# Optimization experiments

Hardware: AMD Instinct MI355X
Metric: run time of the kernel (lower is better)

Reference implementation:

```python
import jax, jax.numpy as jnp
import numpy as np

B, T, D, H = 32, 1024, 512, 512


def setup_inputs() -> dict:
    key = jax.random.key(0)
    ks = jax.random.split(key, 9)
    K = 1.0 / np.sqrt(H)
    u = lambda k, s: jax.random.uniform(k, s, jnp.float32, -K, K)
    return {
        "x": jax.random.normal(ks[0], (B, T, D), jnp.float32),
        "w_ih_fw": u(ks[1], (3 * H, D)),
        "w_hh_fw": u(ks[2], (3 * H, H)),
        "b_ih_fw": u(ks[3], (3 * H,)),
        "b_hh_fw": u(ks[4], (3 * H,)),
        "w_ih_bw": u(ks[5], (3 * H, D)),
        "w_hh_bw": u(ks[6], (3 * H, H)),
        "b_ih_bw": u(ks[7], (3 * H,)),
        "b_hh_bw": u(ks[8], (3 * H,)),
    }


def _gru_scan(x, w_ih, w_hh, b_ih, b_hh, reverse):
    # x: (B, T, D) -> precompute input projections for all steps: (T, B, 3H)
    b, t, d = x.shape
    h_dim = w_hh.shape[1]
    ih = jnp.einsum("btd,gd->tbg", x, w_ih) + b_ih

    def step(h, ih_t):
        hh = h @ w_hh.T + b_hh  # (B, 3H)
        r = jax.nn.sigmoid(ih_t[:, :h_dim] + hh[:, :h_dim])
        z = jax.nn.sigmoid(ih_t[:, h_dim:2 * h_dim] + hh[:, h_dim:2 * h_dim])
        n = jnp.tanh(ih_t[:, 2 * h_dim:] + r * hh[:, 2 * h_dim:])
        h_new = (1.0 - z) * n + z * h
        return h_new, h_new

    h0 = jnp.zeros((b, h_dim), x.dtype)
    h_last, ys = jax.lax.scan(step, h0, ih, reverse=reverse)
    # ys: (T, B, H), aligned to original time indices even when reverse=True
    return jnp.transpose(ys, (1, 0, 2)), h_last


def reference(x, w_ih_fw, w_hh_fw, b_ih_fw, b_hh_fw, w_ih_bw, w_hh_bw, b_ih_bw, b_hh_bw):
    out_fw, h_fw = _gru_scan(x, w_ih_fw, w_hh_fw, b_ih_fw, b_hh_fw, reverse=False)
    out_bw, h_bw = _gru_scan(x, w_ih_bw, w_hh_bw, b_ih_bw, b_hh_bw, reverse=True)
    outputs = jnp.concatenate([out_fw, out_bw], axis=-1)  # (B, T, 2H)
    return outputs, h_fw, h_bw
```

## Files before the change

kernel.cpp:

```cpp
#include <hip/hip_runtime.h>


#define T_LEN 1024
#define B_SZ  32
#define D_SZ  512
#define H_SZ  512
#define NWG_DIR 32
#define JW 16
#define NTHR 512

typedef __attribute__((ext_vector_type(8))) _Float16 half8;
typedef __attribute__((ext_vector_type(4))) float f32x4;
typedef __attribute__((ext_vector_type(4))) int int4v;

__device__ __forceinline__ _Float16 f2h(float f) { return (_Float16)f; }
__device__ __forceinline__ float sigm_f(float v) {
  return __builtin_amdgcn_rcpf(1.f + __expf(-v));
}
__device__ __forceinline__ float tanh_f(float v) {
  return 1.f - 2.f * __builtin_amdgcn_rcpf(1.f + __expf(2.f * v));
}
__device__ __forceinline__ void bar_lgkm() {
  asm volatile("s_waitcnt lgkmcnt(0)\ns_barrier" ::: "memory");
}

__global__ __launch_bounds__(NTHR, 2)
void gru2_persistent(const float* __restrict__ x,
                     const float* __restrict__ wih_fw, const float* __restrict__ whh_fw,
                     const float* __restrict__ bih_fw, const float* __restrict__ bhh_fw,
                     const float* __restrict__ wih_bw, const float* __restrict__ whh_bw,
                     const float* __restrict__ bih_bw, const float* __restrict__ bhh_bw,
                     float* __restrict__ out,
                     unsigned* __restrict__ hexu,
                     unsigned* __restrict__ flags,
                     unsigned* __restrict__ xcdmap,
                     unsigned* __restrict__ gbar,
                     unsigned* __restrict__ slowCnt)
{
  const int bid = blockIdx.x;
  const int dir = bid & 7;
  if (dir >= 2) return;
  const int g = bid >> 3;

  __shared__ float Cp[24 * 272];
  __shared__ float biasLds[96];
  __shared__ int fastSh;

  const int tid  = threadIdx.x;
  const int wave = tid >> 6;
  const int lane = tid & 63;

  const float* wih = dir ? wih_bw : wih_fw;
  const float* whh = dir ? whh_bw : whh_fw;
  const float* bih = dir ? bih_bw : bih_fw;
  const float* bhh = dir ? bhh_bw : bhh_fw;

  if (tid < 48) {
    int grow = (tid >> 4) * H_SZ + g * JW + (tid & 15);
    biasLds[tid]      = bih[grow];
    biasLds[48 + tid] = bhh[grow];
  }

  {
    unsigned xcc;
    asm volatile("s_getreg_b32 %0, hwreg(20, 0, 32)" : "=s"(xcc));
    if (tid == 0)
      __hip_atomic_store(&xcdmap[dir * NWG_DIR + g], xcc + 1u,
                         __ATOMIC_RELAXED, __HIP_MEMORY_SCOPE_AGENT);
    if (wave == 0) {
      unsigned v = 0u; int bud = 1 << 17; bool ok = true;
      for (;;) {
        v = __hip_atomic_load(&xcdmap[lane], __ATOMIC_RELAXED,
                              __HIP_MEMORY_SCOPE_AGENT);
        if (__all(v != 0u)) break;
        if (--bud < 0) { ok = false; break; }
        __builtin_amdgcn_s_sleep(8);
      }
      const unsigned ref0 = __shfl(v, 0);
      const unsigned ref1 = __shfl(v, NWG_DIR);
      const bool uni = __all((lane < NWG_DIR) ? (v == ref0) : (v == ref1));
      if (lane == 0) fastSh = (ok && uni && ref0 != ref1) ? 1 : 0;
    }
  }
  __syncthreads();
  __builtin_amdgcn_fence(__ATOMIC_ACQUIRE, "agent");
  __syncthreads();

  if (tid == 0) {
    if (!fastSh)
      __hip_atomic_fetch_add(slowCnt, 1u, __ATOMIC_RELAXED,
                             __HIP_MEMORY_SCOPE_AGENT);
    asm volatile("s_waitcnt vmcnt(0)" ::: "memory");
    __hip_atomic_fetch_add(gbar, 1u, __ATOMIC_RELAXED, __HIP_MEMORY_SCOPE_AGENT);
    int bud = 1 << 18; bool arrived = true;
    while (__hip_atomic_load(gbar, __ATOMIC_RELAXED,
                             __HIP_MEMORY_SCOPE_AGENT) < 64u) {
      if (--bud < 0) { arrived = false; break; }
      __builtin_amdgcn_s_sleep(4);
    }
    unsigned sv = __hip_atomic_load(slowCnt, __ATOMIC_RELAXED,
                                    __HIP_MEMORY_SCOPE_AGENT);
    fastSh = (arrived && sv == 0u && fastSh) ? 1 : 0;
  }
  __syncthreads();
  const bool fast = (fastSh != 0);

  const bool isHh = (wave >= 4);
  const int  wv   = wave & 3;
  const int  wm   = wv & 1;
  const int  kh   = wv >> 1;

  half8 Bf[3][8];
  {
    const float* W = isHh ? whh : wih;
    #pragma unroll
    for (int gam = 0; gam < 3; ++gam) {
      const int row = gam * H_SZ + g * JW + (lane & 15);
      #pragma unroll
      for (int i = 0; i < 8; ++i) {
        const float* src = W + (size_t)row * D_SZ + (kh * 8 + i) * 32 + ((lane >> 4) << 3);
        float4 v0 = *(const float4*)(src);
        float4 v1 = *(const float4*)(src + 4);
        half8 b;
        b[0]=f2h(v0.x); b[1]=f2h(v0.y); b[2]=f2h(v0.z); b[3]=f2h(v0.w);
        b[4]=f2h(v1.x); b[5]=f2h(v1.y); b[6]=f2h(v1.z); b[7]=f2h(v1.w);
        Bf[gam][i] = b;
      }
    }
  }

  const int arow = wm * 16 + (lane & 15);
  const int koff = (lane >> 4) << 3;
  const float* const xwavebase = x + (size_t)arow * T_LEN * D_SZ + kh * 256 + koff;

  float4 xn[16];
  if (!isHh) {
    const int t0 = dir ? (T_LEN - 1) : 0;
    const float* base = xwavebase + (size_t)t0 * D_SZ;
    #pragma unroll
    for (int i = 0; i < 8; ++i) {
      xn[2*i]   = *(const float4*)(base + i * 32);
      xn[2*i+1] = *(const float4*)(base + i * 32 + 4);
    }
  }
  __syncthreads();

  float hreg = 0.f;
  const int gb = tid >> 4;
  const int gj = tid & 15;
  float* hlast = out + (size_t)B_SZ * T_LEN * (2 * H_SZ) + (size_t)dir * B_SZ * H_SZ;
  const unsigned* const fa = flags + (size_t)dir * NWG_DIR + kh * 16 + (lane & 15);
  int pollbud = 1 << 21;

  for (int s = 0; s < T_LEN; ++s) {
    const int t = dir ? (T_LEN - 1 - s) : s;
    const bool hasNext = (s + 1 < T_LEN);

    f32x4 acc[3] = {{0.f,0.f,0.f,0.f},{0.f,0.f,0.f,0.f},{0.f,0.f,0.f,0.f}};

    if (!isHh) {
      half8 a[8];
      #pragma unroll
      for (int i = 0; i < 8; ++i) {
        float4 u = xn[2*i], w = xn[2*i+1];
        half8 h;
        h[0]=f2h(u.x); h[1]=f2h(u.y); h[2]=f2h(u.z); h[3]=f2h(u.w);
        h[4]=f2h(w.x); h[5]=f2h(w.y); h[6]=f2h(w.z); h[7]=f2h(w.w);
        a[i] = h;
      }
      #pragma unroll
      for (int i = 0; i < 8; ++i)
        #pragma unroll
        for (int gam = 0; gam < 3; ++gam)
          acc[gam] = __builtin_amdgcn_mfma_f32_16x16x32_f16(a[i], Bf[gam][i], acc[gam], 0, 0, 0);
    } else if (s > 0) {
      if (fast) {
        {
          unsigned va, vb;
          asm volatile("global_load_dword %0, %1, off sc0" : "=&v"(va) : "v"(fa));
          asm volatile("global_load_dword %0, %1, off sc0" : "=&v"(vb) : "v"(fa));
          for (;;) {
            asm volatile("s_waitcnt vmcnt(1)" ::: "memory");
            if (__all(va >= (unsigned)s)) break;
            if (--pollbud < 0) break;
            asm volatile("global_load_dword %0, %1, off sc0" : "=&v"(va) : "v"(fa));
            asm volatile("s_waitcnt vmcnt(1)" ::: "memory");
            if (__all(vb >= (unsigned)s)) break;
            if (--pollbud < 0) break;
            asm volatile("global_load_dword %0, %1, off sc0" : "=&v"(vb) : "v"(fa));
          }
          asm volatile("s_waitcnt vmcnt(0)" ::: "memory");
        }
        const char* p0 = (const char*)hexu
            + (((size_t)dir * 2 + ((s - 1) & 1)) * (B_SZ * (H_SZ / 2))) * 4
            + (size_t)arow * (H_SZ * 2) + (size_t)(kh * 256 + koff) * 2;
        int4v hv[8];
        asm volatile(
          "global_load_dwordx4 %0, %8, off sc0\n\t"
          "global_load_dwordx4 %1, %8, off offset:64 sc0\n\t"
          "global_load_dwordx4 %2, %8, off offset:128 sc0\n\t"
          "global_load_dwordx4 %3, %8, off offset:192 sc0\n\t"
          "global_load_dwordx4 %4, %8, off offset:256 sc0\n\t"
          "global_load_dwordx4 %5, %8, off offset:320 sc0\n\t"
          "global_load_dwordx4 %6, %8, off offset:384 sc0\n\t"
          "global_load_dwordx4 %7, %8, off offset:448 sc0\n\t"
          "s_waitcnt vmcnt(0)"
          : "=&v"(hv[0]), "=&v"(hv[1]), "=&v"(hv[2]), "=&v"(hv[3]),
            "=&v"(hv[4]), "=&v"(hv[5]), "=&v"(hv[6]), "=&v"(hv[7])
          : "v"(p0) : "memory");
        __builtin_amdgcn_sched_barrier(0);
        #pragma unroll
        for (int i = 0; i < 8; ++i) {
          half8 a = __builtin_bit_cast(half8, hv[i]);
          #pragma unroll
          for (int gam = 0; gam < 3; ++gam)
            acc[gam] = __builtin_amdgcn_mfma_f32_16x16x32_f16(a, Bf[gam][i], acc[gam], 0, 0, 0);
        }
      } else {
        {
          unsigned va, vb;
          asm volatile("global_load_dword %0, %1, off sc0 sc1" : "=&v"(va) : "v"(fa));
          asm volatile("global_load_dword %0, %1, off sc0 sc1" : "=&v"(vb) : "v"(fa));
          for (;;) {
            asm volatile("s_waitcnt vmcnt(1)" ::: "memory");
            if (__all(va >= (unsigned)s)) break;
            if (--pollbud < 0) break;
            asm volatile("global_load_dword %0, %1, off sc0 sc1" : "=&v"(va) : "v"(fa));
            asm volatile("s_waitcnt vmcnt(1)" ::: "memory");
            if (__all(vb >= (unsigned)s)) break;
            if (--pollbud < 0) break;
            asm volatile("global_load_dword %0, %1, off sc0 sc1" : "=&v"(vb) : "v"(fa));
          }
          asm volatile("s_waitcnt vmcnt(0)" ::: "memory");
        }
        const char* p0 = (const char*)hexu
            + (((size_t)dir * 2 + ((s - 1) & 1)) * (B_SZ * (H_SZ / 2))) * 4
            + (size_t)arow * (H_SZ * 2) + (size_t)(kh * 256 + koff) * 2;
        int4v hv[8];
        asm volatile(
          "global_load_dwordx4 %0, %8, off sc0 sc1\n\t"
          "global_load_dwordx4 %1, %8, off offset:64 sc0 sc1\n\t"
          "global_load_dwordx4 %2, %8, off offset:128 sc0 sc1\n\t"
          "global_load_dwordx4 %3, %8, off offset:192 sc0 sc1\n\t"
          "global_load_dwordx4 %4, %8, off offset:256 sc0 sc1\n\t"
          "global_load_dwordx4 %5, %8, off offset:320 sc0 sc1\n\t"
          "global_load_dwordx4 %6, %8, off offset:384 sc0 sc1\n\t"
          "global_load_dwordx4 %7, %8, off offset:448 sc0 sc1\n\t"
          "s_waitcnt vmcnt(0)"
          : "=&v"(hv[0]), "=&v"(hv[1]), "=&v"(hv[2]), "=&v"(hv[3]),
            "=&v"(hv[4]), "=&v"(hv[5]), "=&v"(hv[6]), "=&v"(hv[7])
          : "v"(p0) : "memory");
        __builtin_amdgcn_sched_barrier(0);
        #pragma unroll
        for (int i = 0; i < 8; ++i) {
          half8 a = __builtin_bit_cast(half8, hv[i]);
          #pragma unroll
          for (int gam = 0; gam < 3; ++gam)
            acc[gam] = __builtin_amdgcn_mfma_f32_16x16x32_f16(a, Bf[gam][i], acc[gam], 0, 0, 0);
        }
      }
    }

    {
      const int src = isHh ? 1 : 0;
      #pragma unroll
      for (int gam = 0; gam < 3; ++gam) {
        float* cp = Cp + (size_t)(((src*2 + kh)*3 + gam)*2 + wm) * 272
                       + ((lane >> 4) << 2) * 17 + (lane & 15);
        #pragma unroll
        for (int vv2 = 0; vv2 < 4; ++vv2) cp[vv2 * 17] = acc[gam][vv2];
      }
    }
    bar_lgkm();

    float hnS;
    {
      const int mb = gb >> 4, rb = gb & 15;
      float sih[3], shh[3];
      #pragma unroll
      for (int gam = 0; gam < 3; ++gam) {
        float aih = 0.f, ahh = 0.f;
        #pragma unroll
        for (int q = 0; q < 2; ++q) {
          aih += Cp[(size_t)(((0*2+q)*3+gam)*2 + mb) * 272 + rb * 17 + gj];
          ahh += Cp[(size_t)(((1*2+q)*3+gam)*2 + mb) * 272 + rb * 17 + gj];
        }
        sih[gam] = aih + biasLds[gam * 16 + gj];
        shh[gam] = ahh + biasLds[48 + gam * 16 + gj];
      }
      const float r = sigm_f(sih[0] + shh[0]);
      const float z = sigm_f(sih[1] + shh[1]);
      const float n = tanh_f(sih[2] + r * shh[2]);
      const float hn = (1.f - z) * n + z * hreg;
      hreg = hn;
      hnS = hn;

      const float hother = __shfl_xor(hn, 1);
      if ((gj & 1) == 0) {
        union { unsigned u; _Float16 h[2]; } pr;
        pr.h[0] = f2h(hn); pr.h[1] = f2h(hother);
        unsigned* hp = hexu + ((size_t)dir * 2 + (s & 1)) * (B_SZ * (H_SZ / 2))
                     + (size_t)gb * (H_SZ / 2) + (g * JW + gj) / 2;
        if (fast)
          asm volatile("global_store_dword %0, %1, off sc0"
                       :: "v"(hp), "v"(pr.u) : "memory");
        else
          __hip_atomic_store(hp, pr.u, __ATOMIC_RELAXED, __HIP_MEMORY_SCOPE_AGENT);
      }
    }
    asm volatile("s_waitcnt vmcnt(0)" ::: "memory");
    bar_lgkm();
    if (tid == 0) {
      unsigned* fp = flags + (size_t)dir * NWG_DIR + g;
      const unsigned fv = (unsigned)(s + 1);
      if (fast)
        asm volatile("global_store_dword %0, %1, off sc0"
                     :: "v"(fp), "v"(fv) : "memory");
      else
        __hip_atomic_store(fp, fv, __ATOMIC_RELAXED, __HIP_MEMORY_SCOPE_AGENT);
    }

    out[((size_t)gb * T_LEN + t) * (2 * H_SZ) + dir * H_SZ + g * JW + gj] = hnS;
    if (s == T_LEN - 1) hlast[gb * H_SZ + g * JW + gj] = hnS;
    if (!isHh && hasNext) {
      const int tn = dir ? (T_LEN - 2 - s) : (s + 1);
      const float* base = xwavebase + (size_t)tn * D_SZ;
      #pragma unroll
      for (int i = 0; i < 8; ++i) {
        xn[2*i]   = *(const float4*)(base + i * 32);
        xn[2*i+1] = *(const float4*)(base + i * 32 + 4);
      }
    }
  }

  __builtin_amdgcn_fence(__ATOMIC_RELEASE, "agent");
}

extern "C" void kernel_launch(void* const* d_in, const int* in_sizes, int n_in,
                              void* d_out, int out_size, void* d_ws, size_t ws_size,
                              hipStream_t stream) {
  const float* x      = (const float*)d_in[0];
  const float* wih_fw = (const float*)d_in[1];
  const float* whh_fw = (const float*)d_in[2];
  const float* bih_fw = (const float*)d_in[3];
  const float* bhh_fw = (const float*)d_in[4];
  const float* wih_bw = (const float*)d_in[5];
  const float* whh_bw = (const float*)d_in[6];
  const float* bih_bw = (const float*)d_in[7];
  const float* bhh_bw = (const float*)d_in[8];
  float* out = (float*)d_out;

  const size_t CTRL_BYTES = 1024;
  const size_t HEX_BYTES  = (size_t)2 * 2 * B_SZ * (H_SZ / 2) * sizeof(unsigned);
  if (ws_size < CTRL_BYTES + HEX_BYTES) return;

  unsigned* xcdmap  = (unsigned*)d_ws;
  unsigned* flags   = (unsigned*)((char*)d_ws + 256);
  unsigned* gbar    = (unsigned*)((char*)d_ws + 512);
  unsigned* slowCnt = (unsigned*)((char*)d_ws + 516);
  unsigned* hexu    = (unsigned*)((char*)d_ws + CTRL_BYTES);

  hipMemsetAsync(d_ws, 0, CTRL_BYTES, stream);
  gru2_persistent<<<dim3(256), dim3(NTHR), 0, stream>>>(
      x, wih_fw, whh_fw, bih_fw, bhh_fw, wih_bw, whh_bw, bih_bw, bhh_bw,
      out, hexu, flags, xcdmap, gbar, slowCnt);
}
```

Before: 3.960 ms.

## Tag exchanged hidden-state words with step generation to validate data in place

Each packed fp16 pair of the exchanged hidden state is now stored as a 64-bit word together with its step number. Consumers reread the h buffer until every word carries the expected generation, which replaces reliance on the per-workgroup flags for data validity. The producer's wait on its stores before the barrier is dropped in the fast path. The cost is twice the exchange traffic, which now has 16 loads per lane instead of 8, plus repeated reloads while polling. The flag poll is still executed before the tagged loads.

New measurement: 5.098 ms. +28.7%, slower.

```diff
diff --git a/kernel.cpp b/kernel.cpp
--- a/kernel.cpp
+++ b/kernel.cpp
@@ -12,6 +12,7 @@
 typedef __attribute__((ext_vector_type(8))) _Float16 half8;
 typedef __attribute__((ext_vector_type(4))) float f32x4;
 typedef __attribute__((ext_vector_type(4))) int int4v;
+typedef __attribute__((ext_vector_type(2))) int int2v;
 
 __device__ __forceinline__ _Float16 f2h(float f) { return (_Float16)f; }
 __device__ __forceinline__ float sigm_f(float v) {
@@ -31,7 +32,7 @@
                      const float* __restrict__ wih_bw, const float* __restrict__ whh_bw,
                      const float* __restrict__ bih_bw, const float* __restrict__ bhh_bw,
                      float* __restrict__ out,
-                     unsigned* __restrict__ hexu,
+                     unsigned long long* __restrict__ hex64,
                      unsigned* __restrict__ flags,
                      unsigned* __restrict__ xcdmap,
                      unsigned* __restrict__ gbar,
@@ -175,89 +176,111 @@
           acc[gam] = __builtin_amdgcn_mfma_f32_16x16x32_f16(a[i], Bf[gam][i], acc[gam], 0, 0, 0);
     } else if (s > 0) {
       if (fast) {
-        {
-          unsigned va, vb;
+        unsigned va, vb;
+        asm volatile("global_load_dword %0, %1, off sc0" : "=&v"(va) : "v"(fa));
+        asm volatile("global_load_dword %0, %1, off sc0" : "=&v"(vb) : "v"(fa));
+        for (;;) {
+          asm volatile("s_waitcnt vmcnt(1)" ::: "memory");
+          if (__all(va >= (unsigned)s)) break;
+          if (--pollbud < 0) break;
           asm volatile("global_load_dword %0, %1, off sc0" : "=&v"(va) : "v"(fa));
+          asm volatile("s_waitcnt vmcnt(1)" ::: "memory");
+          if (__all(vb >= (unsigned)s)) break;
+          if (--pollbud < 0) break;
           asm volatile("global_load_dword %0, %1, off sc0" : "=&v"(vb) : "v"(fa));
-          for (;;) {
-            asm volatile("s_waitcnt vmcnt(1)" ::: "memory");
-            if (__all(va >= (unsigned)s)) break;
-            if (--pollbud < 0) break;
-            asm volatile("global_load_dword %0, %1, off sc0" : "=&v"(va) : "v"(fa));
-            asm volatile("s_waitcnt vmcnt(1)" ::: "memory");
-            if (__all(vb >= (unsigned)s)) break;
-            if (--pollbud < 0) break;
-            asm volatile("global_load_dword %0, %1, off sc0" : "=&v"(vb) : "v"(fa));
-          }
-          asm volatile("s_waitcnt vmcnt(0)" ::: "memory");
-        }
-        const char* p0 = (const char*)hexu
-            + (((size_t)dir * 2 + ((s - 1) & 1)) * (B_SZ * (H_SZ / 2))) * 4
-            + (size_t)arow * (H_SZ * 2) + (size_t)(kh * 256 + koff) * 2;
-        int4v hv[8];
-        asm volatile(
-          "global_load_dwordx4 %0, %8, off sc0\n\t"
-          "global_load_dwordx4 %1, %8, off offset:64 sc0\n\t"
-          "global_load_dwordx4 %2, %8, off offset:128 sc0\n\t"
-          "global_load_dwordx4 %3, %8, off offset:192 sc0\n\t"
-          "global_load_dwordx4 %4, %8, off offset:256 sc0\n\t"
-          "global_load_dwordx4 %5, %8, off offset:320 sc0\n\t"
-          "global_load_dwordx4 %6, %8, off offset:384 sc0\n\t"
-          "global_load_dwordx4 %7, %8, off offset:448 sc0\n\t"
-          "s_waitcnt vmcnt(0)"
-          : "=&v"(hv[0]), "=&v"(hv[1]), "=&v"(hv[2]), "=&v"(hv[3]),
-            "=&v"(hv[4]), "=&v"(hv[5]), "=&v"(hv[6]), "=&v"(hv[7])
-          : "v"(p0) : "memory");
-        __builtin_amdgcn_sched_barrier(0);
-        #pragma unroll
-        for (int i = 0; i < 8; ++i) {
-          half8 a = __builtin_bit_cast(half8, hv[i]);
-          #pragma unroll
-          for (int gam = 0; gam < 3; ++gam)
-            acc[gam] = __builtin_amdgcn_mfma_f32_16x16x32_f16(a, Bf[gam][i], acc[gam], 0, 0, 0);
-        }
+        }
+        asm volatile("s_waitcnt vmcnt(0)" ::: "memory");
       } else {
-        {
-          unsigned va, vb;
+        unsigned va, vb;
+        asm volatile("global_load_dword %0, %1, off sc0 sc1" : "=&v"(va) : "v"(fa));
+        asm volatile("global_load_dword %0, %1, off sc0 sc1" : "=&v"(vb) : "v"(fa));
+        for (;;) {
+          asm volatile("s_waitcnt vmcnt(1)" ::: "memory");
+          if (__all(va >= (unsigned)s)) break;
+          if (--pollbud < 0) break;
           asm volatile("global_load_dword %0, %1, off sc0 sc1" : "=&v"(va) : "v"(fa));
+          asm volatile("s_waitcnt vmcnt(1)" ::: "memory");
+          if (__all(vb >= (unsigned)s)) break;
+          if (--pollbud < 0) break;
           asm volatile("global_load_dword %0, %1, off sc0 sc1" : "=&v"(vb) : "v"(fa));
-          for (;;) {
-            asm volatile("s_waitcnt vmcnt(1)" ::: "memory");
-            if (__all(va >= (unsigned)s)) break;
-            if (--pollbud < 0) break;
-            asm volatile("global_load_dword %0, %1, off sc0 sc1" : "=&v"(va) : "v"(fa));
-            asm volatile("s_waitcnt vmcnt(1)" ::: "memory");
-            if (__all(vb >= (unsigned)s)) break;
-            if (--pollbud < 0) break;
-            asm volatile("global_load_dword %0, %1, off sc0 sc1" : "=&v"(vb) : "v"(fa));
-          }
-          asm volatile("s_waitcnt vmcnt(0)" ::: "memory");
-        }
-        const char* p0 = (const char*)hexu
-            + (((size_t)dir * 2 + ((s - 1) & 1)) * (B_SZ * (H_SZ / 2))) * 4
-            + (size_t)arow * (H_SZ * 2) + (size_t)(kh * 256 + koff) * 2;
-        int4v hv[8];
-        asm volatile(
-          "global_load_dwordx4 %0, %8, off sc0 sc1\n\t"
-          "global_load_dwordx4 %1, %8, off offset:64 sc0 sc1\n\t"
-          "global_load_dwordx4 %2, %8, off offset:128 sc0 sc1\n\t"
-          "global_load_dwordx4 %3, %8, off offset:192 sc0 sc1\n\t"
-          "global_load_dwordx4 %4, %8, off offset:256 sc0 sc1\n\t"
-          "global_load_dwordx4 %5, %8, off offset:320 sc0 sc1\n\t"
-          "global_load_dwordx4 %6, %8, off offset:384 sc0 sc1\n\t"
-          "global_load_dwordx4 %7, %8, off offset:448 sc0 sc1\n\t"
-          "s_waitcnt vmcnt(0)"
-          : "=&v"(hv[0]), "=&v"(hv[1]), "=&v"(hv[2]), "=&v"(hv[3]),
-            "=&v"(hv[4]), "=&v"(hv[5]), "=&v"(hv[6]), "=&v"(hv[7])
-          : "v"(p0) : "memory");
-        __builtin_amdgcn_sched_barrier(0);
-        #pragma unroll
-        for (int i = 0; i < 8; ++i) {
-          half8 a = __builtin_bit_cast(half8, hv[i]);
-          #pragma unroll
-          for (int gam = 0; gam < 3; ++gam)
-            acc[gam] = __builtin_amdgcn_mfma_f32_16x16x32_f16(a, Bf[gam][i], acc[gam], 0, 0, 0);
-        }
+        }
+        asm volatile("s_waitcnt vmcnt(0)" ::: "memory");
+      }
+      const int geni = s;
+      const char* pbase = (const char*)hex64
+          + ((((size_t)dir * 2 + ((s - 1) & 1)) * B_SZ + arow) * 256
+             + (size_t)kh * 128 + (koff >> 1)) * 8;
+      int4v hv[16];
+      for (;;) {
+        if (fast) {
+          asm volatile(
+            "global_load_dwordx4 %0, %16, off sc0\n\t"
+            "global_load_dwordx4 %1, %16, off offset:16 sc0\n\t"
+            "global_load_dwordx4 %2, %16, off offset:128 sc0\n\t"
+            "global_load_dwordx4 %3, %16, off offset:144 sc0\n\t"
+            "global_load_dwordx4 %4, %16, off offset:256 sc0\n\t"
+            "global_load_dwordx4 %5, %16, off offset:272 sc0\n\t"
+            "global_load_dwordx4 %6, %16, off offset:384 sc0\n\t"
+            "global_load_dwordx4 %7, %16, off offset:400 sc0\n\t"
+            "global_load_dwordx4 %8, %16, off offset:512 sc0\n\t"
+            "global_load_dwordx4 %9, %16, off offset:528 sc0\n\t"
+            "global_load_dwordx4 %10, %16, off offset:640 sc0\n\t"
+            "global_load_dwordx4 %11, %16, off offset:656 sc0\n\t"
+            "global_load_dwordx4 %12, %16, off offset:768 sc0\n\t"
+            "global_load_dwordx4 %13, %16, off offset:784 sc0\n\t"
+            "global_load_dwordx4 %14, %16, off offset:896 sc0\n\t"
+            "global_load_dwordx4 %15, %16, off offset:912 sc0\n\t"
+            "s_waitcnt vmcnt(0)"
+            : "=&v"(hv[0]), "=&v"(hv[1]), "=&v"(hv[2]), "=&v"(hv[3]),
+              "=&v"(hv[4]), "=&v"(hv[5]), "=&v"(hv[6]), "=&v"(hv[7]),
+              "=&v"(hv[8]), "=&v"(hv[9]), "=&v"(hv[10]), "=&v"(hv[11]),
+              "=&v"(hv[12]), "=&v"(hv[13]), "=&v"(hv[14]), "=&v"(hv[15])
+            : "v"(pbase)
+            : "memory");
+        } else {
+          asm volatile(
+            "global_load_dwordx4 %0, %16, off sc0 sc1\n\t"
+            "global_load_dwordx4 %1, %16, off offset:16 sc0 sc1\n\t"
+            "global_load_dwordx4 %2, %16, off offset:128 sc0 sc1\n\t"
+            "global_load_dwordx4 %3, %16, off offset:144 sc0 sc1\n\t"
+            "global_load_dwordx4 %4, %16, off offset:256 sc0 sc1\n\t"
+            "global_load_dwordx4 %5, %16, off offset:272 sc0 sc1\n\t"
+            "global_load_dwordx4 %6, %16, off offset:384 sc0 sc1\n\t"
+            "global_load_dwordx4 %7, %16, off offset:400 sc0 sc1\n\t"
+            "global_load_dwordx4 %8, %16, off offset:512 sc0 sc1\n\t"
+            "global_load_dwordx4 %9, %16, off offset:528 sc0 sc1\n\t"
+            "global_load_dwordx4 %10, %16, off offset:640 sc0 sc1\n\t"
+            "global_load_dwordx4 %11, %16, off offset:656 sc0 sc1\n\t"
+            "global_load_dwordx4 %12, %16, off offset:768 sc0 sc1\n\t"
+            "global_load_dwordx4 %13, %16, off offset:784 sc0 sc1\n\t"
+            "global_load_dwordx4 %14, %16, off offset:896 sc0 sc1\n\t"
+            "global_load_dwordx4 %15, %16, off offset:912 sc0 sc1\n\t"
+            "s_waitcnt vmcnt(0)"
+            : "=&v"(hv[0]), "=&v"(hv[1]), "=&v"(hv[2]), "=&v"(hv[3]),
+              "=&v"(hv[4]), "=&v"(hv[5]), "=&v"(hv[6]), "=&v"(hv[7]),
+              "=&v"(hv[8]), "=&v"(hv[9]), "=&v"(hv[10]), "=&v"(hv[11]),
+              "=&v"(hv[12]), "=&v"(hv[13]), "=&v"(hv[14]), "=&v"(hv[15])
+            : "v"(pbase)
+            : "memory");
+        }
+        int bad = 0;
+        #pragma unroll
+        for (int k2 = 0; k2 < 16; ++k2)
+          bad |= (hv[k2][1] ^ geni) | (hv[k2][3] ^ geni);
+        if (__all(bad == 0)) break;
+        if (--pollbud < 0) break;
+        __builtin_amdgcn_s_sleep(1);
+      }
+      __builtin_amdgcn_sched_barrier(0);
+      #pragma unroll
+      for (int i = 0; i < 8; ++i) {
+        int4v w;
+        w[0] = hv[2*i][0];   w[1] = hv[2*i][2];
+        w[2] = hv[2*i+1][0]; w[3] = hv[2*i+1][2];
+        half8 a = __builtin_bit_cast(half8, w);
+        #pragma unroll
+        for (int gam = 0; gam < 3; ++gam)
+          acc[gam] = __builtin_amdgcn_mfma_f32_16x16x32_f16(a, Bf[gam][i], acc[gam], 0, 0, 0);
       }
     }
 
@@ -299,16 +322,21 @@
       if ((gj & 1) == 0) {
         union { unsigned u; _Float16 h[2]; } pr;
         pr.h[0] = f2h(hn); pr.h[1] = f2h(hother);
-        unsigned* hp = hexu + ((size_t)dir * 2 + (s & 1)) * (B_SZ * (H_SZ / 2))
-                     + (size_t)gb * (H_SZ / 2) + (g * JW + gj) / 2;
-        if (fast)
-          asm volatile("global_store_dword %0, %1, off sc0"
-                       :: "v"(hp), "v"(pr.u) : "memory");
-        else
-          __hip_atomic_store(hp, pr.u, __ATOMIC_RELAXED, __HIP_MEMORY_SCOPE_AGENT);
-      }
-    }
-    asm volatile("s_waitcnt vmcnt(0)" ::: "memory");
+        unsigned long long* hp = hex64
+            + ((size_t)dir * 2 + (s & 1)) * (B_SZ * 256)
+            + (size_t)gb * 256 + (g * 8 + (gj >> 1));
+        if (fast) {
+          int2v pk; pk[0] = (int)pr.u; pk[1] = (int)(s + 1);
+          asm volatile("global_store_dwordx2 %0, %1, off sc0"
+                       :: "v"(hp), "v"(pk) : "memory");
+        } else {
+          const unsigned long long pk64 =
+              (unsigned long long)pr.u | ((unsigned long long)(unsigned)(s + 1) << 32);
+          __hip_atomic_store(hp, pk64, __ATOMIC_RELAXED, __HIP_MEMORY_SCOPE_AGENT);
+        }
+      }
+    }
+    if (!fast) asm volatile("s_waitcnt vmcnt(0)" ::: "memory");
     bar_lgkm();
     if (tid == 0) {
       unsigned* fp = flags + (size_t)dir * NWG_DIR + g;
@@ -351,17 +379,17 @@
   float* out = (float*)d_out;
 
   const size_t CTRL_BYTES = 1024;
-  const size_t HEX_BYTES  = (size_t)2 * 2 * B_SZ * (H_SZ / 2) * sizeof(unsigned);
+  const size_t HEX_BYTES  = (size_t)2 * 2 * B_SZ * 256 * sizeof(unsigned long long);
   if (ws_size < CTRL_BYTES + HEX_BYTES) return;
 
   unsigned* xcdmap  = (unsigned*)d_ws;
   unsigned* flags   = (unsigned*)((char*)d_ws + 256);
   unsigned* gbar    = (unsigned*)((char*)d_ws + 512);
   unsigned* slowCnt = (unsigned*)((char*)d_ws + 516);
-  unsigned* hexu    = (unsigned*)((char*)d_ws + CTRL_BYTES);
+  unsigned long long* hex64 = (unsigned long long*)((char*)d_ws + CTRL_BYTES);
 
   hipMemsetAsync(d_ws, 0, CTRL_BYTES, stream);
   gru2_persistent<<<dim3(256), dim3(NTHR), 0, stream>>>(
       x, wih_fw, whh_fw, bih_fw, bhh_fw, wih_bw, whh_bw, bih_bw, bhh_bw,
-      out, hexu, flags, xcdmap, gbar, slowCnt);
-}
+      out, hex64, flags, xcdmap, gbar, slowCnt);
+}
```

## Move gate epilogue to hh waves and prefetch next x before MFMA

Applied to the files above, without the earlier changes.

The gate nonlinearity and state update are now computed only by the 256 hh-role threads, each handling two batch rows (b and b+16). The ih waves skip the epilogue and the vmcnt wait. The next timestep's x load is issued right after the fp16 conversion and before the MFMAs, so it overlaps with compute instead of sitting at the end of the step. This aims to shorten the critical path of each recurrent step and free the ih waves to run ahead, at the cost of doubling the epilogue work per hh thread.

After: 4.444 ms. 1.12x slower.

```diff
diff --git a/kernel.cpp b/kernel.cpp
--- a/kernel.cpp
+++ b/kernel.cpp
@@ -145,9 +145,10 @@
   }
   __syncthreads();
 
-  float hreg = 0.f;
-  const int gb = tid >> 4;
-  const int gj = tid & 15;
+  const int q   = tid - 256;
+  const int gb0 = (q >> 4) & 15;
+  const int gj2 = q & 15;
+  float hreg0 = 0.f, hreg1 = 0.f;
   float* hlast = out + (size_t)B_SZ * T_LEN * (2 * H_SZ) + (size_t)dir * B_SZ * H_SZ;
   const unsigned* const fa = flags + (size_t)dir * NWG_DIR + kh * 16 + (lane & 15);
   int pollbud = 1 << 21;
@@ -167,6 +168,15 @@
         h[0]=f2h(u.x); h[1]=f2h(u.y); h[2]=f2h(u.z); h[3]=f2h(u.w);
         h[4]=f2h(w.x); h[5]=f2h(w.y); h[6]=f2h(w.z); h[7]=f2h(w.w);
         a[i] = h;
+      }
+      if (hasNext) {
+        const int tn = dir ? (T_LEN - 2 - s) : (s + 1);
+        const float* base = xwavebase + (size_t)tn * D_SZ;
+        #pragma unroll
+        for (int i = 0; i < 8; ++i) {
+          xn[2*i]   = *(const float4*)(base + i * 32);
+          xn[2*i+1] = *(const float4*)(base + i * 32 + 4);
+        }
       }
       #pragma unroll
       for (int i = 0; i < 8; ++i)
@@ -273,42 +283,52 @@
     }
     bar_lgkm();
 
-    float hnS;
-    {
-      const int mb = gb >> 4, rb = gb & 15;
-      float sih[3], shh[3];
-      #pragma unroll
-      for (int gam = 0; gam < 3; ++gam) {
-        float aih = 0.f, ahh = 0.f;
-        #pragma unroll
-        for (int q = 0; q < 2; ++q) {
-          aih += Cp[(size_t)(((0*2+q)*3+gam)*2 + mb) * 272 + rb * 17 + gj];
-          ahh += Cp[(size_t)(((1*2+q)*3+gam)*2 + mb) * 272 + rb * 17 + gj];
-        }
-        sih[gam] = aih + biasLds[gam * 16 + gj];
-        shh[gam] = ahh + biasLds[48 + gam * 16 + gj];
-      }
-      const float r = sigm_f(sih[0] + shh[0]);
-      const float z = sigm_f(sih[1] + shh[1]);
-      const float n = tanh_f(sih[2] + r * shh[2]);
-      const float hn = (1.f - z) * n + z * hreg;
-      hreg = hn;
-      hnS = hn;
-
-      const float hother = __shfl_xor(hn, 1);
-      if ((gj & 1) == 0) {
-        union { unsigned u; _Float16 h[2]; } pr;
-        pr.h[0] = f2h(hn); pr.h[1] = f2h(hother);
-        unsigned* hp = hexu + ((size_t)dir * 2 + (s & 1)) * (B_SZ * (H_SZ / 2))
-                     + (size_t)gb * (H_SZ / 2) + (g * JW + gj) / 2;
-        if (fast)
+    float hn0S = 0.f, hn1S = 0.f;
+    if (isHh) {
+      #pragma unroll
+      for (int half = 0; half < 2; ++half) {
+        const int mb = half;
+        const int rb = gb0;
+        float sih[3], shh[3];
+        #pragma unroll
+        for (int gam = 0; gam < 3; ++gam) {
+          float aih = 0.f, ahh = 0.f;
+          #pragma unroll
+          for (int qk = 0; qk < 2; ++qk) {
+            aih += Cp[(size_t)(((0*2+qk)*3+gam)*2 + mb) * 272 + rb * 17 + gj2];
+            ahh += Cp[(size_t)(((1*2+qk)*3+gam)*2 + mb) * 272 + rb * 17 + gj2];
+          }
+          sih[gam] = aih + biasLds[gam * 16 + gj2];
+          shh[gam] = ahh + biasLds[48 + gam * 16 + gj2];
+        }
+        const float r = sigm_f(sih[0] + shh[0]);
+        const float z = sigm_f(sih[1] + shh[1]);
+        const float n = tanh_f(sih[2] + r * shh[2]);
+        const float hprev = half ? hreg1 : hreg0;
+        const float hn = (1.f - z) * n + z * hprev;
+        if (half) { hreg1 = hn; hn1S = hn; } else { hreg0 = hn; hn0S = hn; }
+      }
+      const float ho0 = __shfl_xor(hn0S, 1);
+      const float ho1 = __shfl_xor(hn1S, 1);
+      if ((gj2 & 1) == 0) {
+        union { unsigned u; _Float16 h[2]; } p0u, p1u;
+        p0u.h[0] = f2h(hn0S); p0u.h[1] = f2h(ho0);
+        p1u.h[0] = f2h(hn1S); p1u.h[1] = f2h(ho1);
+        const size_t pb = ((size_t)dir * 2 + (s & 1)) * (B_SZ * (H_SZ / 2));
+        unsigned* hp0 = hexu + pb + (size_t)gb0 * (H_SZ / 2) + g * 8 + (gj2 >> 1);
+        unsigned* hp1 = hexu + pb + (size_t)(gb0 + 16) * (H_SZ / 2) + g * 8 + (gj2 >> 1);
+        if (fast) {
           asm volatile("global_store_dword %0, %1, off sc0"
-                       :: "v"(hp), "v"(pr.u) : "memory");
-        else
-          __hip_atomic_store(hp, pr.u, __ATOMIC_RELAXED, __HIP_MEMORY_SCOPE_AGENT);
-      }
-    }
-    asm volatile("s_waitcnt vmcnt(0)" ::: "memory");
+                       :: "v"(hp0), "v"(p0u.u) : "memory");
+          asm volatile("global_store_dword %0, %1, off sc0"
+                       :: "v"(hp1), "v"(p1u.u) : "memory");
+        } else {
+          __hip_atomic_store(hp0, p0u.u, __ATOMIC_RELAXED, __HIP_MEMORY_SCOPE_AGENT);
+          __hip_atomic_store(hp1, p1u.u, __ATOMIC_RELAXED, __HIP_MEMORY_SCOPE_AGENT);
+        }
+      }
+      asm volatile("s_waitcnt vmcnt(0)" ::: "memory");
+    }
     bar_lgkm();
     if (tid == 0) {
       unsigned* fp = flags + (size_t)dir * NWG_DIR + g;
@@ -320,15 +340,12 @@
         __hip_atomic_store(fp, fv, __ATOMIC_RELAXED, __HIP_MEMORY_SCOPE_AGENT);
     }
 
-    out[((size_t)gb * T_LEN + t) * (2 * H_SZ) + dir * H_SZ + g * JW + gj] = hnS;
-    if (s == T_LEN - 1) hlast[gb * H_SZ + g * JW + gj] = hnS;
-    if (!isHh && hasNext) {
-      const int tn = dir ? (T_LEN - 2 - s) : (s + 1);
-      const float* base = xwavebase + (size_t)tn * D_SZ;
-      #pragma unroll
-      for (int i = 0; i < 8; ++i) {
-        xn[2*i]   = *(const float4*)(base + i * 32);
-        xn[2*i+1] = *(const float4*)(base + i * 32 + 4);
+    if (isHh) {
+      out[((size_t)gb0 * T_LEN + t) * (2 * H_SZ) + dir * H_SZ + g * JW + gj2] = hn0S;
+      out[((size_t)(gb0 + 16) * T_LEN + t) * (2 * H_SZ) + dir * H_SZ + g * JW + gj2] = hn1S;
+      if (s == T_LEN - 1) {
+        hlast[gb0 * H_SZ + g * JW + gj2] = hn0S;
+        hlast[(gb0 + 16) * H_SZ + g * JW + gj2] = hn1S;
       }
     }
   }
```
